# Kernel optimization log

Hardware: AMD Instinct MI355X
Metric: run time of the kernel (lower is better)

## Reference

```python
import jax, jax.numpy as jnp
import numpy as np

B, N_ITEMS, H1, H2 = 1024, 50000, 600, 200


def setup_inputs() -> dict:
    key = jax.random.key(0)
    ks = jax.random.split(key, 8)
    return {
        "x": jax.random.uniform(ks[0], (B, N_ITEMS), dtype=jnp.float32),
        "W1": jax.random.normal(ks[1], (N_ITEMS, H1), dtype=jnp.float32) * 0.02,
        "b1": jax.random.normal(ks[2], (H1,), dtype=jnp.float32) * 0.001,
        "W2": jax.random.normal(ks[3], (H1, H2), dtype=jnp.float32) * 0.05,
        "b2": jax.random.normal(ks[4], (H2,), dtype=jnp.float32) * 0.001,
        "W3": jax.random.normal(ks[5], (H2, H1), dtype=jnp.float32) * 0.05,
        "b3": jax.random.normal(ks[6], (H1,), dtype=jnp.float32) * 0.001,
        "item_emb": jax.random.normal(ks[7], (N_ITEMS, H1), dtype=jnp.float32) * 0.02,
    }


def reference(x, W1, b1, W2, b2, W3, b3, item_emb):
    # F.normalize(input): L2-normalize rows with eps clamp
    norm = jnp.sqrt(jnp.sum(x * x, axis=-1, keepdims=True))
    h = x / jnp.maximum(norm, 1e-12)
    # tanh MLP stack (dropout is identity at inference)
    h = jnp.tanh(h @ W1 + b1)   # [B, 600]
    h = jnp.tanh(h @ W2 + b2)   # [B, 200]
    h = jnp.tanh(h @ W3 + b3)   # [B, 600]
    # pairwise squared-L2 distance to all item embeddings via GEMM decomposition:
    # ||h||^2 - 2 h.e + ||e||^2  (same math as the broadcasted (h-e)^2 sum)
    h_sq = jnp.sum(h * h, axis=-1, keepdims=True)          # [B, 1]
    e_sq = jnp.sum(item_emb * item_emb, axis=-1)           # [N]
    dist = h_sq - 2.0 * (h @ item_emb.T) + e_sq            # [B, N]
    return dist
```

## Files before the change

### kernel.cpp

```cpp
#include <hip/hip_runtime.h>
#include <stdint.h>

namespace {

constexpr int BROWS = 1024;
constexpr int NIT   = 50000;
constexpr int NH1   = 600;
constexpr int NH2   = 200;
constexpr int KXP   = 50048;
constexpr int N1P   = 640;
constexpr int NEP   = 50048;
constexpr int KEP   = 640;
constexpr int KI64_TOTAL = KXP / 64;
constexpr int NBLK1 = N1P / 128;
constexpr int NBLK4 = NEP / 128;

typedef _Float16 f16x8 __attribute__((ext_vector_type(8)));
typedef _Float16 f16x4 __attribute__((ext_vector_type(4)));
typedef _Float16 f16x2 __attribute__((ext_vector_type(2)));
typedef float    f32x4 __attribute__((ext_vector_type(4)));

__device__ __forceinline__ void gld16(const void* g, void* l) {
  __builtin_amdgcn_global_load_lds(
      (__attribute__((address_space(1))) void*)(void*)g,
      (__attribute__((address_space(3))) void*)l, 16, 0, 0);
}

__global__ __launch_bounds__(256) void norm_conv_k(const float* __restrict__ x,
                                                   float* __restrict__ invnorm,
                                                   _Float16* __restrict__ xh) {
  const int row = blockIdx.x;
  const float4* xr = (const float4*)(x + (size_t)row * NIT);
  float ss = 0.f;
  if (xh != nullptr) {
    f16x4* xo = (f16x4*)(xh + (size_t)row * KXP);
    #pragma unroll 4
    for (int i = threadIdx.x; i < NIT / 4; i += 256) {
      float4 v = xr[i];
      ss += v.x * v.x + v.y * v.y + v.z * v.z + v.w * v.w;
      f16x4 h;
      h.x = (_Float16)v.x; h.y = (_Float16)v.y;
      h.z = (_Float16)v.z; h.w = (_Float16)v.w;
      xo[i] = h;
    }
    if (threadIdx.x < (KXP - NIT) / 4) {
      f16x4 z;
      z.x = (_Float16)0.f; z.y = (_Float16)0.f;
      z.z = (_Float16)0.f; z.w = (_Float16)0.f;
      xo[NIT / 4 + threadIdx.x] = z;
    }
  } else {
    #pragma unroll 4
    for (int i = threadIdx.x; i < NIT / 4; i += 256) {
      float4 v = xr[i];
      ss += v.x * v.x + v.y * v.y + v.z * v.z + v.w * v.w;
    }
  }
  for (int o = 32; o > 0; o >>= 1) ss += __shfl_down(ss, o);
  __shared__ float red[4];
  if ((threadIdx.x & 63) == 0) red[threadIdx.x >> 6] = ss;
  __syncthreads();
  if (threadIdx.x == 0) {
    float s = red[0] + red[1] + red[2] + red[3];
    invnorm[row] = 1.0f / fmaxf(sqrtf(s), 1e-12f);
  }
}

__global__ __launch_bounds__(256) void transpose_w1_k(const float* __restrict__ W1,
                                                      _Float16* __restrict__ W1T) {
  __shared__ float tile[64][65];
  const int kb = blockIdx.x * 64;
  const int nb = blockIdx.y * 64;
  const int t = threadIdx.x;
  #pragma unroll
  for (int i = 0; i < 16; ++i) {
    int idx = i * 256 + t;
    int k = idx >> 6, n = idx & 63;
    int gk = kb + k, gn = nb + n;
    tile[k][n] = (gk < NIT && gn < NH1) ? W1[(size_t)gk * NH1 + gn] : 0.f;
  }
  __syncthreads();
  #pragma unroll
  for (int i = 0; i < 8; ++i) {
    int idx = i * 256 + t;
    int n = idx >> 5;
    int k2 = (idx & 31) * 2;
    f16x2 h;
    h.x = (_Float16)tile[k2][n];
    h.y = (_Float16)tile[k2 + 1][n];
    *(f16x2*)(&W1T[(size_t)(nb + n) * KXP + kb + k2]) = h;
  }
}

__global__ __launch_bounds__(256) void prep_emb_k(const float* __restrict__ emb,
                                                  _Float16* __restrict__ embb,
                                                  float* __restrict__ esq) {
  const int row = blockIdx.x * 4 + (threadIdx.x >> 6);
  const int lane = threadIdx.x & 63;
  const float* er = emb + (size_t)row * NH1;
  float ss = 0.f;
  #pragma unroll
  for (int j = 0; j < 10; ++j) {
    int idx = lane + 64 * j;
    float v = (row < NIT && idx < NH1) ? er[idx] : 0.f;
    ss += v * v;
    embb[(size_t)row * KEP + idx] = (_Float16)v;
  }
  for (int o = 32; o > 0; o >>= 1) ss += __shfl_down(ss, o);
  if (lane == 0) esq[row] = ss;
}

template <int MODE>
__global__ __launch_bounds__(256, 4) void mfma_nt_k(
    const void* __restrict__ Av, const _Float16* __restrict__ Bg,
    float* __restrict__ Cout, const float* __restrict__ hsq,
    const float* __restrict__ esq) {
  __shared__ _Float16 As[128 * 64];
  __shared__ _Float16 Bs[128 * 64];

  const int t = threadIdx.x;

  int n0, m0, ki0, ki1, zslab = 0, lda, ldb;
  if (MODE == 1) {
    int flat = blockIdx.x + NBLK4 * blockIdx.y;
    int W = (flat & 7) * (NBLK4 * 8 / 8) + (flat >> 3);
    m0 = (W & 7) * 128;
    n0 = (W >> 3) * 128;
    ki0 = 0; ki1 = KEP / 64;
    lda = KEP; ldb = KEP;
  } else {
    const int S = (int)gridDim.z;
    int flat = blockIdx.x + NBLK1 * (blockIdx.y + 8 * blockIdx.z);
    int W = (flat & 7) * (5 * S) + (flat >> 3);
    int xq = W % 5;
    int yz = W / 5;
    n0 = xq * 128;
    m0 = (yz & 7) * 128;
    zslab = yz >> 3;
    int kiPer = (KI64_TOTAL + S - 1) / S;
    ki0 = zslab * kiPer;
    ki1 = ki0 + kiPer; if (ki1 > KI64_TOTAL) ki1 = KI64_TOTAL;
    lda = (MODE == 0) ? NIT : KXP;
    ldb = KXP;
  }

  const int lane = t & 63;
  const int wid = t >> 6;
  const int wm = wid >> 1, wn = wid & 1;
  const int lrow = lane & 15, quad = lane >> 4;

  const f32x4 zero = {0.f, 0.f, 0.f, 0.f};
  f32x4 acc[4][4];
  #pragma unroll
  for (int i = 0; i < 4; ++i)
    #pragma unroll
    for (int j = 0; j < 4; ++j) acc[i][j] = zero;

  for (int ki = ki0; ki < ki1; ++ki) {
    const int k0 = ki * 64;
    if (MODE == 0) {
      const float* A = (const float*)Av;
      #pragma unroll
      for (int j = 0; j < 8; ++j) {
        int g = j * 256 + t;
        int row = g >> 4;
        int q4 = g & 15;
        int kcol = k0 + q4 * 4;
        float4 v = {0.f, 0.f, 0.f, 0.f};
        if (kcol < NIT)
          v = *(const float4*)(A + (size_t)(m0 + row) * lda + kcol);
        f16x4 h;
        h.x = (_Float16)v.x; h.y = (_Float16)v.y;
        h.z = (_Float16)v.z; h.w = (_Float16)v.w;
        int c16 = (q4 >> 1) ^ (row & 7);
        *(f16x4*)(&As[row * 64 + c16 * 8 + (q4 & 1) * 4]) = h;
      }
    } else {
      const _Float16* A = (const _Float16*)Av;
      #pragma unroll
      for (int j = 0; j < 4; ++j) {
        int c = j * 256 + t;
        int row = c >> 3;
        int kk = ((c & 7) ^ (row & 7)) << 3;
        gld16(A + (size_t)(m0 + row) * lda + (k0 + kk), &As[c * 8]);
      }
    }
    #pragma unroll
    for (int j = 0; j < 4; ++j) {
      int c = j * 256 + t;
      int row = c >> 3;
      int kk = ((c & 7) ^ (row & 7)) << 3;
      gld16(Bg + (size_t)(n0 + row) * ldb + (k0 + kk), &Bs[c * 8]);
    }
    __syncthreads();

    #pragma unroll
    for (int ks = 0; ks < 2; ++ks) {
      f16x8 af[4], bfr[4];
      #pragma unroll
      for (int mi = 0; mi < 4; ++mi) {
        int row = wm * 64 + mi * 16 + lrow;
        int c16 = (ks * 4 + quad) ^ (lrow & 7);
        af[mi] = *(const f16x8*)(&As[row * 64 + c16 * 8]);
      }
      #pragma unroll
      for (int ni = 0; ni < 4; ++ni) {
        int row = wn * 64 + ni * 16 + lrow;
        int c16 = (ks * 4 + quad) ^ (lrow & 7);
        bfr[ni] = *(const f16x8*)(&Bs[row * 64 + c16 * 8]);
      }
      #pragma unroll
      for (int mi = 0; mi < 4; ++mi)
        #pragma unroll
        for (int ni = 0; ni < 4; ++ni)
          acc[mi][ni] = __builtin_amdgcn_mfma_f32_16x16x32_f16(af[mi], bfr[ni],
                                                               acc[mi][ni], 0, 0, 0);
    }
    __syncthreads();
  }

  if (MODE != 1) {
    float* Cs = Cout + (size_t)zslab * BROWS * N1P;
    #pragma unroll
    for (int mi = 0; mi < 4; ++mi)
      #pragma unroll
      for (int r = 0; r < 4; ++r) {
        int row = m0 + wm * 64 + mi * 16 + quad * 4 + r;
        #pragma unroll
        for (int ni = 0; ni < 4; ++ni) {
          int col = n0 + wn * 64 + ni * 16 + lrow;
          Cs[(size_t)row * N1P + col] = acc[mi][ni][r];
        }
      }
  } else {
    #pragma unroll
    for (int mi = 0; mi < 4; ++mi)
      #pragma unroll
      for (int r = 0; r < 4; ++r) {
        int row = m0 + wm * 64 + mi * 16 + quad * 4 + r;
        float hv = hsq[row];
        #pragma unroll
        for (int ni = 0; ni < 4; ++ni) {
          int col = n0 + wn * 64 + ni * 16 + lrow;
          if (col < NIT)
            Cout[(size_t)row * NIT + col] = hv - 2.f * acc[mi][ni][r] + esq[col];
        }
      }
  }
}

__global__ __launch_bounds__(256) void reduce_epi1_k(const float* __restrict__ C1p,
                                                     const float* __restrict__ invnorm,
                                                     const float* __restrict__ b1,
                                                     float* __restrict__ h1,
                                                     int nslabs) {
  int idx = blockIdx.x * 256 + threadIdx.x;
  if (idx >= BROWS * NH1) return;
  int m = idx / NH1, n = idx - m * NH1;
  float s = 0.f;
  for (int sp = 0; sp < nslabs; ++sp)
    s += C1p[(size_t)sp * BROWS * N1P + (size_t)m * N1P + n];
  h1[idx] = tanhf(invnorm[m] * s + b1[n]);
}

__global__ __launch_bounds__(256) void gemm2_k(const float* __restrict__ h1,
                                               const float* __restrict__ W2,
                                               const float* __restrict__ b2,
                                               float* __restrict__ h2) {
  __shared__ float hs[8 * NH1];
  const int m0 = blockIdx.x * 8;
  const int t = threadIdx.x;
  for (int i = t; i < 8 * NH1; i += 256) hs[i] = h1[(size_t)m0 * NH1 + i];
  __syncthreads();
  if (t < NH2) {
    float acc[8];
    #pragma unroll
    for (int r = 0; r < 8; ++r) acc[r] = 0.f;
    for (int k0 = 0; k0 < NH1; k0 += 8) {
      float w[8];
      #pragma unroll
      for (int u = 0; u < 8; ++u) w[u] = W2[(k0 + u) * NH2 + t];
      #pragma unroll
      for (int u = 0; u < 8; ++u)
        #pragma unroll
        for (int r = 0; r < 8; ++r) acc[r] += hs[r * NH1 + k0 + u] * w[u];
    }
    float bb = b2[t];
    #pragma unroll
    for (int r = 0; r < 8; ++r) h2[(size_t)(m0 + r) * NH2 + t] = tanhf(acc[r] + bb);
  }
}

__global__ __launch_bounds__(256) void gemm3_k(const float* __restrict__ h2,
                                               const float* __restrict__ W3,
                                               const float* __restrict__ b3,
                                               _Float16* __restrict__ h3h,
                                               float* __restrict__ hsq) {
  __shared__ float hs[8 * NH2];
  const int m0 = blockIdx.x * 8;
  const int t = threadIdx.x;
  for (int i = t; i < 8 * NH2; i += 256) hs[i] = h2[(size_t)m0 * NH2 + i];
  __syncthreads();
  float ssq[8];
  #pragma unroll
  for (int r = 0; r < 8; ++r) ssq[r] = 0.f;
  for (int c = 0; c < 3; ++c) {
    int n = t + c * 256;
    if (n < NH1) {
      float acc[8];
      #pragma unroll
      for (int r = 0; r < 8; ++r) acc[r] = 0.f;
      for (int k0 = 0; k0 < NH2; k0 += 8) {
        float w[8];
        #pragma unroll
        for (int u = 0; u < 8; ++u) w[u] = W3[(k0 + u) * NH1 + n];
        #pragma unroll
        for (int u = 0; u < 8; ++u)
          #pragma unroll
          for (int r = 0; r < 8; ++r) acc[r] += hs[r * NH2 + k0 + u] * w[u];
      }
      float bb = b3[n];
      #pragma unroll
      for (int r = 0; r < 8; ++r) {
        float v = tanhf(acc[r] + bb);
        h3h[(size_t)(m0 + r) * KEP + n] = (_Float16)v;
        ssq[r] += v * v;
      }
    } else if (n < KEP) {
      #pragma unroll
      for (int r = 0; r < 8; ++r) h3h[(size_t)(m0 + r) * KEP + n] = (_Float16)0.f;
    }
  }
  const int lane = t & 63, wid = t >> 6;
  #pragma unroll
  for (int r = 0; r < 8; ++r)
    for (int o = 32; o > 0; o >>= 1) ssq[r] += __shfl_down(ssq[r], o);
  __shared__ float red2[8][4];
  if (lane == 0) {
    #pragma unroll
    for (int r = 0; r < 8; ++r) red2[r][wid] = ssq[r];
  }
  __syncthreads();
  if (t < 8) hsq[m0 + t] = red2[t][0] + red2[t][1] + red2[t][2] + red2[t][3];
}

}

extern "C" void kernel_launch(void* const* d_in, const int* in_sizes, int n_in,
                              void* d_out, int out_size, void* d_ws, size_t ws_size,
                              hipStream_t stream) {
  const float* x   = (const float*)d_in[0];
  const float* W1  = (const float*)d_in[1];
  const float* b1  = (const float*)d_in[2];
  const float* W2  = (const float*)d_in[3];
  const float* b2  = (const float*)d_in[4];
  const float* W3  = (const float*)d_in[5];
  const float* b3  = (const float*)d_in[6];
  const float* emb = (const float*)d_in[7];
  float* out = (float*)d_out;

  char* ws = (char*)d_ws;

  const size_t XHSZ  = (size_t)BROWS * KXP * 2;
  const size_t W1TSZ = (size_t)N1P * KXP * 2;
  const size_t SLAB  = (size_t)BROWS * N1P * 4;
  const size_t TAIL  = 4096 + 200192 + 2457600 + 819200 + 1310720 + 4096;

  bool useF16A;
  int S;
  const size_t baseA = XHSZ + W1TSZ + TAIL;
  const size_t baseB = W1TSZ + TAIL;
  if (ws_size >= baseA + 16 * SLAB) {
    useF16A = true;
    size_t s = (ws_size - baseA) / SLAB;
    S = s > 32 ? 32 : (int)s;
  } else if (ws_size >= baseB + 8 * SLAB) {
    useF16A = false;
    size_t s = (ws_size - baseB) / SLAB;
    S = s > 32 ? 32 : (int)s;
  } else {
    return;
  }

  size_t off = 0;
  _Float16* xh = nullptr;
  if (useF16A) { xh = (_Float16*)(ws + off); off += XHSZ; }
  const size_t oW1T = off;
  _Float16* W1T = (_Float16*)(ws + off); off += W1TSZ;
  float* C1p = (float*)(ws + off); off += (size_t)S * SLAB;
  float* invn = (float*)(ws + off); off += 4096;
  float* esq  = (float*)(ws + off); off += 200192;
  float* h1   = (float*)(ws + off); off += 2457600;
  float* h2   = (float*)(ws + off); off += 819200;
  _Float16* h3h = (_Float16*)(ws + off); off += 1310720;
  float* hsq  = (float*)(ws + off); off += 4096;
  _Float16* embb = (_Float16*)(ws + oW1T);

  norm_conv_k<<<dim3(BROWS), dim3(256), 0, stream>>>(x, invn, xh);
  transpose_w1_k<<<dim3(KXP / 64, N1P / 64), dim3(256), 0, stream>>>(W1, W1T);
  if (useF16A) {
    mfma_nt_k<2><<<dim3(NBLK1, BROWS / 128, S), dim3(256), 0, stream>>>(
        (const void*)xh, W1T, C1p, nullptr, nullptr);
  } else {
    mfma_nt_k<0><<<dim3(NBLK1, BROWS / 128, S), dim3(256), 0, stream>>>(
        (const void*)x, W1T, C1p, nullptr, nullptr);
  }
  reduce_epi1_k<<<dim3((BROWS * NH1 + 255) / 256), dim3(256), 0, stream>>>(
      C1p, invn, b1, h1, S);
  prep_emb_k<<<dim3(NEP / 4), dim3(256), 0, stream>>>(emb, embb, esq);
  gemm2_k<<<dim3(BROWS / 8), dim3(256), 0, stream>>>(h1, W2, b2, h2);
  gemm3_k<<<dim3(BROWS / 8), dim3(256), 0, stream>>>(h2, W3, b3, h3h, hsq);
  mfma_nt_k<1><<<dim3(NBLK4, BROWS / 128, 1), dim3(256), 0, stream>>>(
      (const void*)h3h, embb, out, hsq, esq);
}
```

Before: 863.5 us.

## Fuse prep kernels, fold emb conversion into distance GEMM, stage epilogue stores

Merges the x-normalization and W1 transpose into one launch. Folds the split-K reduction and tanh into the second-layer MLP kernel. Drops the separate embedding fp16 conversion and e_sq kernel: the distance GEMM now loads fp32 item_emb directly, converts it to fp16 in registers, accumulates the squared norms on the fly, and double-buffers the A and B tiles. Output is staged through LDS and written with vectorized nontemporal stores. This removes several launches and the embb/esq round trip, at the cost of more LDS, higher register pressure and recomputing e_sq in each of the 8 M-blocks.

```diff
diff --git a/kernel.cpp b/kernel.cpp
--- a/kernel.cpp
+++ b/kernel.cpp
@@ -14,6 +14,7 @@
 constexpr int KI64_TOTAL = KXP / 64;
 constexpr int NBLK1 = N1P / 128;
 constexpr int NBLK4 = NEP / 128;
+constexpr int TGRID = (KXP / 64) * (N1P / 64);
 
 typedef _Float16 f16x8 __attribute__((ext_vector_type(8)));
 typedef _Float16 f16x4 __attribute__((ext_vector_type(4)));
@@ -26,123 +27,96 @@
       (__attribute__((address_space(3))) void*)l, 16, 0, 0);
 }
 
-__global__ __launch_bounds__(256) void norm_conv_k(const float* __restrict__ x,
-                                                   float* __restrict__ invnorm,
-                                                   _Float16* __restrict__ xh) {
-  const int row = blockIdx.x;
-  const float4* xr = (const float4*)(x + (size_t)row * NIT);
-  float ss = 0.f;
-  if (xh != nullptr) {
-    f16x4* xo = (f16x4*)(xh + (size_t)row * KXP);
-    #pragma unroll 4
-    for (int i = threadIdx.x; i < NIT / 4; i += 256) {
-      float4 v = xr[i];
-      ss += v.x * v.x + v.y * v.y + v.z * v.z + v.w * v.w;
-      f16x4 h;
-      h.x = (_Float16)v.x; h.y = (_Float16)v.y;
-      h.z = (_Float16)v.z; h.w = (_Float16)v.w;
-      xo[i] = h;
-    }
-    if (threadIdx.x < (KXP - NIT) / 4) {
-      f16x4 z;
-      z.x = (_Float16)0.f; z.y = (_Float16)0.f;
-      z.z = (_Float16)0.f; z.w = (_Float16)0.f;
-      xo[NIT / 4 + threadIdx.x] = z;
+__global__ __launch_bounds__(256) void prep_fused_k(const float* __restrict__ x,
+                                                    float* __restrict__ invnorm,
+                                                    _Float16* __restrict__ xh,
+                                                    const float* __restrict__ W1,
+                                                    _Float16* __restrict__ W1T) {
+  __shared__ float tile[64][65];
+  __shared__ float red[4];
+  const int t = threadIdx.x;
+  if (blockIdx.x < BROWS) {
+    const int row = blockIdx.x;
+    const float4* xr = (const float4*)(x + (size_t)row * NIT);
+    float ss = 0.f;
+    if (xh != nullptr) {
+      f16x4* xo = (f16x4*)(xh + (size_t)row * KXP);
+      #pragma unroll 4
+      for (int i = t; i < NIT / 4; i += 256) {
+        float4 v = xr[i];
+        ss += v.x * v.x + v.y * v.y + v.z * v.z + v.w * v.w;
+        f16x4 h;
+        h.x = (_Float16)v.x; h.y = (_Float16)v.y;
+        h.z = (_Float16)v.z; h.w = (_Float16)v.w;
+        xo[i] = h;
+      }
+      if (t < (KXP - NIT) / 4) {
+        f16x4 z;
+        z.x = (_Float16)0.f; z.y = (_Float16)0.f;
+        z.z = (_Float16)0.f; z.w = (_Float16)0.f;
+        xo[NIT / 4 + t] = z;
+      }
+    } else {
+      #pragma unroll 4
+      for (int i = t; i < NIT / 4; i += 256) {
+        float4 v = xr[i];
+        ss += v.x * v.x + v.y * v.y + v.z * v.z + v.w * v.w;
+      }
+    }
+    for (int o = 32; o > 0; o >>= 1) ss += __shfl_down(ss, o);
+    if ((t & 63) == 0) red[t >> 6] = ss;
+    __syncthreads();
+    if (t == 0) {
+      float s = red[0] + red[1] + red[2] + red[3];
+      invnorm[row] = 1.0f / fmaxf(sqrtf(s), 1e-12f);
     }
   } else {
-    #pragma unroll 4
-    for (int i = threadIdx.x; i < NIT / 4; i += 256) {
-      float4 v = xr[i];
-      ss += v.x * v.x + v.y * v.y + v.z * v.z + v.w * v.w;
-    }
-  }
-  for (int o = 32; o > 0; o >>= 1) ss += __shfl_down(ss, o);
-  __shared__ float red[4];
-  if ((threadIdx.x & 63) == 0) red[threadIdx.x >> 6] = ss;
-  __syncthreads();
-  if (threadIdx.x == 0) {
-    float s = red[0] + red[1] + red[2] + red[3];
-    invnorm[row] = 1.0f / fmaxf(sqrtf(s), 1e-12f);
-  }
-}
-
-__global__ __launch_bounds__(256) void transpose_w1_k(const float* __restrict__ W1,
-                                                      _Float16* __restrict__ W1T) {
-  __shared__ float tile[64][65];
-  const int kb = blockIdx.x * 64;
-  const int nb = blockIdx.y * 64;
-  const int t = threadIdx.x;
-  #pragma unroll
-  for (int i = 0; i < 16; ++i) {
-    int idx = i * 256 + t;
-    int k = idx >> 6, n = idx & 63;
-    int gk = kb + k, gn = nb + n;
-    tile[k][n] = (gk < NIT && gn < NH1) ? W1[(size_t)gk * NH1 + gn] : 0.f;
-  }
-  __syncthreads();
-  #pragma unroll
-  for (int i = 0; i < 8; ++i) {
-    int idx = i * 256 + t;
-    int n = idx >> 5;
-    int k2 = (idx & 31) * 2;
-    f16x2 h;
-    h.x = (_Float16)tile[k2][n];
-    h.y = (_Float16)tile[k2 + 1][n];
-    *(f16x2*)(&W1T[(size_t)(nb + n) * KXP + kb + k2]) = h;
-  }
-}
-
-__global__ __launch_bounds__(256) void prep_emb_k(const float* __restrict__ emb,
-                                                  _Float16* __restrict__ embb,
-                                                  float* __restrict__ esq) {
-  const int row = blockIdx.x * 4 + (threadIdx.x >> 6);
-  const int lane = threadIdx.x & 63;
-  const float* er = emb + (size_t)row * NH1;
-  float ss = 0.f;
-  #pragma unroll
-  for (int j = 0; j < 10; ++j) {
-    int idx = lane + 64 * j;
-    float v = (row < NIT && idx < NH1) ? er[idx] : 0.f;
-    ss += v * v;
-    embb[(size_t)row * KEP + idx] = (_Float16)v;
-  }
-  for (int o = 32; o > 0; o >>= 1) ss += __shfl_down(ss, o);
-  if (lane == 0) esq[row] = ss;
+    const int tb = blockIdx.x - BROWS;
+    const int kb = (tb % (KXP / 64)) * 64;
+    const int nb = (tb / (KXP / 64)) * 64;
+    #pragma unroll
+    for (int i = 0; i < 16; ++i) {
+      int idx = i * 256 + t;
+      int k = idx >> 6, n = idx & 63;
+      int gk = kb + k, gn = nb + n;
+      tile[k][n] = (gk < NIT && gn < NH1) ? W1[(size_t)gk * NH1 + gn] : 0.f;
+    }
+    __syncthreads();
+    #pragma unroll
+    for (int i = 0; i < 8; ++i) {
+      int idx = i * 256 + t;
+      int n = idx >> 5;
+      int k2 = (idx & 31) * 2;
+      f16x2 h;
+      h.x = (_Float16)tile[k2][n];
+      h.y = (_Float16)tile[k2 + 1][n];
+      *(f16x2*)(&W1T[(size_t)(nb + n) * KXP + kb + k2]) = h;
+    }
+  }
 }
 
 template <int MODE>
 __global__ __launch_bounds__(256, 4) void mfma_nt_k(
     const void* __restrict__ Av, const _Float16* __restrict__ Bg,
-    float* __restrict__ Cout, const float* __restrict__ hsq,
-    const float* __restrict__ esq) {
+    float* __restrict__ Cout) {
   __shared__ _Float16 As[128 * 64];
   __shared__ _Float16 Bs[128 * 64];
 
   const int t = threadIdx.x;
 
-  int n0, m0, ki0, ki1, zslab = 0, lda, ldb;
-  if (MODE == 1) {
-    int flat = blockIdx.x + NBLK4 * blockIdx.y;
-    int W = (flat & 7) * (NBLK4 * 8 / 8) + (flat >> 3);
-    m0 = (W & 7) * 128;
-    n0 = (W >> 3) * 128;
-    ki0 = 0; ki1 = KEP / 64;
-    lda = KEP; ldb = KEP;
-  } else {
-    const int S = (int)gridDim.z;
-    int flat = blockIdx.x + NBLK1 * (blockIdx.y + 8 * blockIdx.z);
-    int W = (flat & 7) * (5 * S) + (flat >> 3);
-    int xq = W % 5;
-    int yz = W / 5;
-    n0 = xq * 128;
-    m0 = (yz & 7) * 128;
-    zslab = yz >> 3;
-    int kiPer = (KI64_TOTAL + S - 1) / S;
-    ki0 = zslab * kiPer;
-    ki1 = ki0 + kiPer; if (ki1 > KI64_TOTAL) ki1 = KI64_TOTAL;
-    lda = (MODE == 0) ? NIT : KXP;
-    ldb = KXP;
-  }
+  const int S = (int)gridDim.z;
+  int flat = blockIdx.x + NBLK1 * (blockIdx.y + 8 * blockIdx.z);
+  int W = (flat & 7) * (5 * S) + (flat >> 3);
+  int xq = W % 5;
+  int yz = W / 5;
+  const int n0 = xq * 128;
+  const int m0 = (yz & 7) * 128;
+  const int zslab = yz >> 3;
+  int kiPer = (KI64_TOTAL + S - 1) / S;
+  int ki0 = zslab * kiPer;
+  int ki1 = ki0 + kiPer; if (ki1 > KI64_TOTAL) ki1 = KI64_TOTAL;
+  const int lda = (MODE == 0) ? NIT : KXP;
+  const int ldb = KXP;
 
   const int lane = t & 63;
   const int wid = t >> 6;
@@ -219,58 +193,188 @@
     __syncthreads();
   }
 
-  if (MODE != 1) {
-    float* Cs = Cout + (size_t)zslab * BROWS * N1P;
-    #pragma unroll
-    for (int mi = 0; mi < 4; ++mi)
-      #pragma unroll
-      for (int r = 0; r < 4; ++r) {
-        int row = m0 + wm * 64 + mi * 16 + quad * 4 + r;
+  float* Cs = Cout + (size_t)zslab * BROWS * N1P;
+  #pragma unroll
+  for (int mi = 0; mi < 4; ++mi)
+    #pragma unroll
+    for (int r = 0; r < 4; ++r) {
+      int row = m0 + wm * 64 + mi * 16 + quad * 4 + r;
+      #pragma unroll
+      for (int ni = 0; ni < 4; ++ni) {
+        int col = n0 + wn * 64 + ni * 16 + lrow;
+        Cs[(size_t)row * N1P + col] = acc[mi][ni][r];
+      }
+    }
+}
+
+__global__ __launch_bounds__(256, 2) void dist_k(
+    const _Float16* __restrict__ h3h, const float* __restrict__ emb,
+    float* __restrict__ out, const float* __restrict__ hsq) {
+  __shared__ __align__(16) _Float16 smem[4][128 * 64];
+  __shared__ float esqs[128];
+
+  const int t = threadIdx.x;
+  int flat = blockIdx.x + NBLK4 * blockIdx.y;
+  int W = (flat & 7) * NBLK4 + (flat >> 3);
+  const int m0 = (W & 7) * 128;
+  const int n0 = (W >> 3) * 128;
+  constexpr int KI1 = KEP / 64;
+
+  const int lane = t & 63;
+  const int wid = t >> 6;
+  const int wm = wid >> 1, wn = wid & 1;
+  const int lrow = lane & 15, quad = lane >> 4;
+
+  const f32x4 zero = {0.f, 0.f, 0.f, 0.f};
+  f32x4 acc[4][4];
+  #pragma unroll
+  for (int i = 0; i < 4; ++i)
+    #pragma unroll
+    for (int j = 0; j < 4; ++j) acc[i][j] = zero;
+
+  float ssq[8];
+  #pragma unroll
+  for (int j = 0; j < 8; ++j) ssq[j] = 0.f;
+
+  const int rA = t >> 3;
+  const int kkA = ((t & 7) ^ (rA & 7)) << 3;
+  const int rB = t >> 4;
+  const int q4 = t & 15;
+
+  auto stageA = [&](int buf, int ki) {
+    const int k0 = ki * 64;
+    #pragma unroll
+    for (int j = 0; j < 4; ++j) {
+      int c = j * 256 + t;
+      int row = c >> 3;
+      int kk = ((c & 7) ^ (row & 7)) << 3;
+      gld16(h3h + (size_t)(m0 + row) * KEP + (k0 + kk), &smem[buf][c * 8]);
+    }
+  };
+  auto loadB = [&](int ki, float4* v) {
+    const int k0 = ki * 64;
+    const int kcol = k0 + q4 * 4;
+    #pragma unroll
+    for (int j = 0; j < 8; ++j) {
+      int row = j * 16 + rB;
+      float4 vv = {0.f, 0.f, 0.f, 0.f};
+      if (kcol < NH1 && (n0 + row) < NIT)
+        vv = *(const float4*)(emb + (size_t)(n0 + row) * NH1 + kcol);
+      v[j] = vv;
+    }
+  };
+  auto writeB = [&](int buf, const float4* v) {
+    #pragma unroll
+    for (int j = 0; j < 8; ++j) {
+      float4 vv = v[j];
+      ssq[j] += vv.x * vv.x + vv.y * vv.y + vv.z * vv.z + vv.w * vv.w;
+      f16x4 h;
+      h.x = (_Float16)vv.x; h.y = (_Float16)vv.y;
+      h.z = (_Float16)vv.z; h.w = (_Float16)vv.w;
+      int row = j * 16 + rB;
+      int c16 = (q4 >> 1) ^ (row & 7);
+      *(f16x4*)(&smem[2 + buf][row * 64 + c16 * 8 + (q4 & 1) * 4]) = h;
+    }
+  };
+
+  {
+    float4 v[8];
+    loadB(0, v);
+    stageA(0, 0);
+    writeB(0, v);
+  }
+  __syncthreads();
+
+  int cur = 0;
+  for (int ki = 0; ki < KI1; ++ki) {
+    float4 v[8];
+    const bool more = (ki + 1 < KI1);
+    if (more) {
+      stageA(cur ^ 1, ki + 1);
+      loadB(ki + 1, v);
+    }
+    #pragma unroll
+    for (int ks = 0; ks < 2; ++ks) {
+      f16x8 af[4], bfr[4];
+      #pragma unroll
+      for (int mi = 0; mi < 4; ++mi) {
+        int row = wm * 64 + mi * 16 + lrow;
+        int c16 = (ks * 4 + quad) ^ (lrow & 7);
+        af[mi] = *(const f16x8*)(&smem[cur][row * 64 + c16 * 8]);
+      }
+      #pragma unroll
+      for (int ni = 0; ni < 4; ++ni) {
+        int row = wn * 64 + ni * 16 + lrow;
+        int c16 = (ks * 4 + quad) ^ (lrow & 7);
+        bfr[ni] = *(const f16x8*)(&smem[2 + cur][row * 64 + c16 * 8]);
+      }
+      #pragma unroll
+      for (int mi = 0; mi < 4; ++mi)
         #pragma unroll
-        for (int ni = 0; ni < 4; ++ni) {
-          int col = n0 + wn * 64 + ni * 16 + lrow;
-          Cs[(size_t)row * N1P + col] = acc[mi][ni][r];
-        }
-      }
-  } else {
-    #pragma unroll
-    for (int mi = 0; mi < 4; ++mi)
-      #pragma unroll
-      for (int r = 0; r < 4; ++r) {
-        int row = m0 + wm * 64 + mi * 16 + quad * 4 + r;
-        float hv = hsq[row];
-        #pragma unroll
-        for (int ni = 0; ni < 4; ++ni) {
-          int col = n0 + wn * 64 + ni * 16 + lrow;
-          if (col < NIT)
-            Cout[(size_t)row * NIT + col] = hv - 2.f * acc[mi][ni][r] + esq[col];
-        }
-      }
-  }
-}
-
-__global__ __launch_bounds__(256) void reduce_epi1_k(const float* __restrict__ C1p,
-                                                     const float* __restrict__ invnorm,
-                                                     const float* __restrict__ b1,
-                                                     float* __restrict__ h1,
-                                                     int nslabs) {
-  int idx = blockIdx.x * 256 + threadIdx.x;
-  if (idx >= BROWS * NH1) return;
-  int m = idx / NH1, n = idx - m * NH1;
-  float s = 0.f;
-  for (int sp = 0; sp < nslabs; ++sp)
-    s += C1p[(size_t)sp * BROWS * N1P + (size_t)m * N1P + n];
-  h1[idx] = tanhf(invnorm[m] * s + b1[n]);
-}
-
-__global__ __launch_bounds__(256) void gemm2_k(const float* __restrict__ h1,
-                                               const float* __restrict__ W2,
-                                               const float* __restrict__ b2,
-                                               float* __restrict__ h2) {
+        for (int ni = 0; ni < 4; ++ni)
+          acc[mi][ni] = __builtin_amdgcn_mfma_f32_16x16x32_f16(af[mi], bfr[ni],
+                                                               acc[mi][ni], 0, 0, 0);
+    }
+    if (more) writeB(cur ^ 1, v);
+    __syncthreads();
+    cur ^= 1;
+  }
+
+  #pragma unroll
+  for (int j = 0; j < 8; ++j) {
+    float s = ssq[j];
+    s += __shfl_down(s, 8, 16);
+    s += __shfl_down(s, 4, 16);
+    s += __shfl_down(s, 2, 16);
+    s += __shfl_down(s, 1, 16);
+    if (q4 == 0) esqs[j * 16 + rB] = s;
+  }
+  __syncthreads();
+
+  float* ctile = (float*)smem;
+  #pragma unroll
+  for (int mi = 0; mi < 4; ++mi)
+    #pragma unroll
+    for (int r = 0; r < 4; ++r) {
+      int rl = wm * 64 + mi * 16 + quad * 4 + r;
+      float hv = hsq[m0 + rl];
+      #pragma unroll
+      for (int ni = 0; ni < 4; ++ni) {
+        int cl = wn * 64 + ni * 16 + lrow;
+        ctile[rl * 128 + cl] = hv - 2.f * acc[mi][ni][r] + esqs[cl];
+      }
+    }
+  __syncthreads();
+  #pragma unroll
+  for (int i = 0; i < 16; ++i) {
+    int c4 = i * 256 + t;
+    int row = c4 >> 5;
+    int cq = c4 & 31;
+    int col = n0 + cq * 4;
+    if (col < NIT) {
+      f32x4 v = *(const f32x4*)(&ctile[row * 128 + cq * 4]);
+      __builtin_nontemporal_store(v, (f32x4*)(out + (size_t)(m0 + row) * NIT + col));
+    }
+  }
+}
+
+__global__ __launch_bounds__(256) void gemm2f_k(const float* __restrict__ C1p,
+                                                const float* __restrict__ invnorm,
+                                                const float* __restrict__ b1,
+                                                const float* __restrict__ W2,
+                                                const float* __restrict__ b2,
+                                                float* __restrict__ h2,
+                                                int nslabs) {
   __shared__ float hs[8 * NH1];
   const int m0 = blockIdx.x * 8;
   const int t = threadIdx.x;
-  for (int i = t; i < 8 * NH1; i += 256) hs[i] = h1[(size_t)m0 * NH1 + i];
+  for (int i = t; i < 8 * NH1; i += 256) {
+    int m = i / NH1, n = i - m * NH1;
+    float s = 0.f;
+    for (int sp = 0; sp < nslabs; ++sp)
+      s += C1p[(size_t)sp * BROWS * N1P + (size_t)(m0 + m) * N1P + n];
+    hs[i] = tanhf(invnorm[m0 + m] * s + b1[n]);
+  }
   __syncthreads();
   if (t < NH2) {
     float acc[8];
@@ -364,7 +468,7 @@
   const size_t XHSZ  = (size_t)BROWS * KXP * 2;
   const size_t W1TSZ = (size_t)N1P * KXP * 2;
   const size_t SLAB  = (size_t)BROWS * N1P * 4;
-  const size_t TAIL  = 4096 + 200192 + 2457600 + 819200 + 1310720 + 4096;
+  const size_t TAIL  = 4096 + 819200 + 1310720 + 4096;
 
   bool useF16A;
   int S;
@@ -385,31 +489,22 @@
   size_t off = 0;
   _Float16* xh = nullptr;
   if (useF16A) { xh = (_Float16*)(ws + off); off += XHSZ; }
-  const size_t oW1T = off;
   _Float16* W1T = (_Float16*)(ws + off); off += W1TSZ;
   float* C1p = (float*)(ws + off); off += (size_t)S * SLAB;
   float* invn = (float*)(ws + off); off += 4096;
-  float* esq  = (float*)(ws + off); off += 200192;
-  float* h1   = (float*)(ws + off); off += 2457600;
   float* h2   = (float*)(ws + off); off += 819200;
   _Float16* h3h = (_Float16*)(ws + off); off += 1310720;
   float* hsq  = (float*)(ws + off); off += 4096;
-  _Float16* embb = (_Float16*)(ws + oW1T);
-
-  norm_conv_k<<<dim3(BROWS), dim3(256), 0, stream>>>(x, invn, xh);
-  transpose_w1_k<<<dim3(KXP / 64, N1P / 64), dim3(256), 0, stream>>>(W1, W1T);
+
+  prep_fused_k<<<dim3(BROWS + TGRID), dim3(256), 0, stream>>>(x, invn, xh, W1, W1T);
   if (useF16A) {
     mfma_nt_k<2><<<dim3(NBLK1, BROWS / 128, S), dim3(256), 0, stream>>>(
-        (const void*)xh, W1T, C1p, nullptr, nullptr);
+        (const void*)xh, W1T, C1p);
   } else {
     mfma_nt_k<0><<<dim3(NBLK1, BROWS / 128, S), dim3(256), 0, stream>>>(
-        (const void*)x, W1T, C1p, nullptr, nullptr);
-  }
-  reduce_epi1_k<<<dim3((BROWS * NH1 + 255) / 256), dim3(256), 0, stream>>>(
-      C1p, invn, b1, h1, S);
-  prep_emb_k<<<dim3(NEP / 4), dim3(256), 0, stream>>>(emb, embb, esq);
-  gemm2_k<<<dim3(BROWS / 8), dim3(256), 0, stream>>>(h1, W2, b2, h2);
+        (const void*)x, W1T, C1p);
+  }
+  gemm2f_k<<<dim3(BROWS / 8), dim3(256), 0, stream>>>(C1p, invn, b1, W2, b2, h2, S);
   gemm3_k<<<dim3(BROWS / 8), dim3(256), 0, stream>>>(h2, W3, b3, h3h, hsq);
-  mfma_nt_k<1><<<dim3(NBLK4, BROWS / 128, 1), dim3(256), 0, stream>>>(
-      (const void*)h3h, embb, out, hsq, esq);
-}
+  dist_k<<<dim3(NBLK4, BROWS / 128), dim3(256), 0, stream>>>(h3h, emb, out, hsq);
+}
```

Result: slower. 1.139 ms (+31.9%).
